# Performance work log

Hardware: AMD Instinct MI355X
Metric: run time of the kernel (lower is better)

Reference implementation:

```python
import jax, jax.numpy as jnp
import numpy as np

DIM = 512
DIM_INNER = 512
NUM_HEADS = 16
HEAD_DIM = DIM_INNER // NUM_HEADS  # 32


def setup_inputs() -> dict:
    key = jax.random.key(0)
    k1, k2, k3, k4 = jax.random.split(key, 4)
    b, n = 1, 4096
    x = jax.random.normal(k1, (b, n, DIM), dtype=jnp.float32)
    # torch nn.Linear weights, stored as (in, out) so y = x @ W (+ b)
    s_qkv = 1.0 / np.sqrt(DIM)
    W_qkv = jax.random.uniform(k2, (DIM, DIM_INNER * 3), jnp.float32, -s_qkv, s_qkv)
    W_a = jax.random.uniform(k3, (DIM, NUM_HEADS * 2), jnp.float32, -s_qkv, s_qkv)
    b_a = jax.random.uniform(k4, (NUM_HEADS * 2,), jnp.float32, -s_qkv, s_qkv)
    return {"x": x, "W_qkv": W_qkv, "W_a": W_a, "b_a": b_a}


def _gate_loop(q, k, v, a):
    # q,k,v: (bh, n, d) float32; a: (bh, n, 1, 1) complex64
    kv = jnp.einsum('bnd,bne->bnde', k, v).astype(jnp.complex64)  # (bh, n, d, d)

    def binop(ei, ej):
        a_i, kv_i = ei
        a_j, kv_j = ej
        return a_j * a_i, a_j * kv_i + kv_j

    _, kv = jax.lax.associative_scan(binop, (a, kv), axis=1)
    return jnp.einsum('bnd,bnde->bne', q, kv.real)


def reference(x, W_qkv, W_a, b_a):
    b, n, _ = x.shape
    h, d = NUM_HEADS, HEAD_DIM

    qkv = x @ W_qkv                                   # (b, n, 3*dim_inner)
    q, k, v = jnp.split(qkv, 3, axis=-1)

    def to_heads(t):  # 'b n (h d) -> (b h) n d'
        return t.reshape(b, n, h, d).transpose(0, 2, 1, 3).reshape(b * h, n, d)

    q, k, v = map(to_heads, (q, k, v))

    a_lin = x @ W_a + b_a                             # (b, n, 2h)
    a_ri = a_lin.reshape(b, n, h, 2)
    a_c = jax.lax.complex(a_ri[..., 0], a_ri[..., 1])  # (b, n, h)
    mag = jnp.abs(a_c)
    ph = jnp.angle(a_c)
    gate = jax.lax.complex(jnp.cos(ph), jnp.sin(ph)) * jax.nn.sigmoid(mag).astype(jnp.complex64)
    gate = gate.transpose(0, 2, 1).reshape(b * h, n, 1, 1)  # '(b h) n 1 1'

    out = _gate_loop(q, k, v, gate)                   # (bh, n, d)
    out = out.reshape(b, h, n, d).transpose(0, 2, 1, 3).reshape(b, n, h * d)
    # out_proj is Identity since dim_inner == dim
    return out
```

## Files before the change

kernel.cpp:

```cpp
#include <hip/hip_runtime.h>
#include <hip/hip_bf16.h>

#define SEQ    4096
#define DIM    512
#define DIM3   1536
#define NH     16
#define HD     32
#define CHUNK  64
#define NCHUNK (SEQ / CHUNK)

typedef __attribute__((ext_vector_type(8))) short short8;
typedef __attribute__((ext_vector_type(4))) float f32x4;
typedef __attribute__((ext_vector_type(4))) unsigned short u16x4;
typedef __attribute__((ext_vector_type(4))) unsigned int u32x4;

__device__ inline unsigned short f2bf(float f) {
  unsigned u = __builtin_bit_cast(unsigned, f);
  unsigned r = (u + 0x7fff + ((u >> 16) & 1)) >> 16;
  return (unsigned short)r;
}
__device__ inline float bf2f(unsigned short b) {
  unsigned u = ((unsigned)b) << 16;
  return __builtin_bit_cast(float, u);
}

__global__ __launch_bounds__(256) void gl_cvt_gate(
    const float* __restrict__ x, const float* __restrict__ W,
    const float* __restrict__ Wa, const float* __restrict__ ba,
    unsigned short* __restrict__ xb, unsigned short* __restrict__ Wt,
    float2* __restrict__ graw) {
  __shared__ union {
    float wtile[32][33];
    struct { float xs[4][DIM]; float red[4][8][32]; } g;
  } sm;
  int b = blockIdx.x;
  if (b < 2048) {
    int i = b * 256 + threadIdx.x;
    float4 v = ((const float4*)x)[i];
    u16x4 o = {f2bf(v.x), f2bf(v.y), f2bf(v.z), f2bf(v.w)};
    ((u16x4*)xb)[i] = o;
  } else if (b < 2816) {
    b -= 2048;
    int bx = b % 48, by = b / 48;
    int tx = threadIdx.x & 31, ty = threadIdx.x >> 5;
    for (int i = ty; i < 32; i += 8)
      sm.wtile[i][tx] = W[(size_t)(by * 32 + i) * DIM3 + bx * 32 + tx];
    __syncthreads();
    for (int i = ty; i < 32; i += 8)
      Wt[(size_t)(bx * 32 + i) * DIM + by * 32 + tx] = f2bf(sm.wtile[tx][i]);
  } else {
    const int n0 = (b - 2816) * 4;
    const int tid = threadIdx.x;
    const float4* xv = (const float4*)(x + (size_t)n0 * DIM);
    float4* xsv = (float4*)&sm.g.xs[0][0];
    for (int i = tid; i < 512; i += 256) xsv[i] = xv[i];
    __syncthreads();
    const int o = tid & 31, s = tid >> 5;
    float pr[4] = {0, 0, 0, 0};
    for (int k = s * 64; k < s * 64 + 64; ++k) {
      float w = Wa[k * 32 + o];
      #pragma unroll
      for (int r = 0; r < 4; ++r) pr[r] += sm.g.xs[r][k] * w;
    }
    #pragma unroll
    for (int r = 0; r < 4; ++r) sm.g.red[r][s][o] = pr[r];
    __syncthreads();
    if (tid < 128) {
      int r = tid >> 5, oo = tid & 31;
      float acc = ba[oo];
      #pragma unroll
      for (int ss = 0; ss < 8; ++ss) acc += sm.g.red[r][ss][oo];
      sm.g.red[r][0][oo] = acc;
    }
    __syncthreads();
    if (tid < 64) {
      int r = tid >> 4, hh = tid & 15;
      float re = sm.g.red[r][0][2 * hh], im = sm.g.red[r][0][2 * hh + 1];
      float mag = sqrtf(re * re + im * im);
      float lml = -log1pf(expf(-mag));
      float ph = atan2f(im, re);
      graw[(size_t)hh * SEQ + n0 + r] = make_float2(lml, ph);
    }
  }
}

#define GBM 128
#define GBN 128
#define GBK 64
__global__ __launch_bounds__(256) void gl_gemm_mfma(
    const unsigned short* __restrict__ A, const unsigned short* __restrict__ Bt,
    unsigned short* __restrict__ C) {
  __shared__ unsigned short As[2][GBM * GBK];
  __shared__ unsigned short Bs[2][GBM * GBK];
  const int tid = threadIdx.x;
  const int id = blockIdx.x;
  const int tile = (id & 7) * 48 + (id >> 3);
  const int by = tile / 12, bx = tile % 12;
  const int row0 = by * GBM, col0 = bx * GBN;
  const int wid = tid >> 6, lane = tid & 63;
  const int wr = wid >> 1, wc = wid & 1;
  const int lr = lane & 15, lg = lane >> 4;

  auto stage = [&](int buf, int t) {
    const int k0 = t * GBK;
    #pragma unroll
    for (int i = 0; i < 4; ++i) {
      int byteoff = i * 4096 + tid * 16;
      int row = byteoff >> 7;
      int logslot = ((byteoff >> 4) & 7) ^ (row & 7);
      const unsigned short* gp = A + (size_t)(row0 + row) * DIM + k0 + logslot * 8;
      __builtin_amdgcn_global_load_lds(
          (const __attribute__((address_space(1))) void*)gp,
          (__attribute__((address_space(3))) void*)((char*)As[buf] + byteoff),
          16, 0, 0);
    }
    #pragma unroll
    for (int i = 0; i < 4; ++i) {
      int byteoff = i * 4096 + tid * 16;
      int row = byteoff >> 7;
      int logslot = ((byteoff >> 4) & 7) ^ (row & 7);
      const unsigned short* gp = Bt + (size_t)(col0 + row) * DIM + k0 + logslot * 8;
      __builtin_amdgcn_global_load_lds(
          (const __attribute__((address_space(1))) void*)gp,
          (__attribute__((address_space(3))) void*)((char*)Bs[buf] + byteoff),
          16, 0, 0);
    }
  };

  f32x4 acc[4][4] = {};
  stage(0, 0);

  #pragma unroll
  for (int t = 0; t < 8; ++t) {
    const int p = t & 1;
    if (t < 7) {
      stage(p ^ 1, t + 1);
      asm volatile("s_waitcnt vmcnt(8)" ::: "memory");
    } else {
      asm volatile("s_waitcnt vmcnt(0)" ::: "memory");
    }
    __syncthreads();
    const char* AsB = (const char*)As[p];
    const char* BsB = (const char*)Bs[p];
    #pragma unroll
    for (int ks = 0; ks < 2; ++ks) {
      short8 af[4], bfr[4];
      #pragma unroll
      for (int m = 0; m < 4; ++m) {
        int row = wr * 64 + m * 16 + lr;
        int ps = (ks * 4 + lg) ^ (row & 7);
        af[m] = *(const short8*)(AsB + row * 128 + ps * 16);
      }
      #pragma unroll
      for (int n = 0; n < 4; ++n) {
        int col = wc * 64 + n * 16 + lr;
        int ps = (ks * 4 + lg) ^ (col & 7);
        bfr[n] = *(const short8*)(BsB + col * 128 + ps * 16);
      }
      #pragma unroll
      for (int m = 0; m < 4; ++m)
        #pragma unroll
        for (int n = 0; n < 4; ++n)
          acc[m][n] = __builtin_amdgcn_mfma_f32_16x16x32_bf16(
              af[m], bfr[n], acc[m][n], 0, 0, 0);
    }
    __syncthreads();
  }

  #pragma unroll
  for (int m = 0; m < 4; ++m)
    #pragma unroll
    for (int n = 0; n < 4; ++n) {
      int grow0 = row0 + wr * 64 + m * 16 + lg * 4;
      int gcol = col0 + wc * 64 + n * 16 + lr;
      #pragma unroll
      for (int j = 0; j < 4; ++j)
        C[(size_t)(grow0 + j) * DIM3 + gcol] = f2bf(acc[m][n][j]);
    }
}

__global__ __launch_bounds__(128) void gl_pass1(
    const unsigned short* __restrict__ qkv, const float2* __restrict__ graw,
    float2* __restrict__ LmPh, float* __restrict__ SLre,
    float* __restrict__ SLim, float2* __restrict__ Aprod) {
  const int b = blockIdx.x;
  const int c = b & (NCHUNK - 1), h = b >> 6;
  const int tid = threadIdx.x, w = tid >> 6, lane = tid & 63;
  const int lr = lane & 15, lg = lane >> 4;
  const int n0 = c * CHUNK;
  __shared__ float2 lmph[CHUNK];

  float2 g = graw[(size_t)h * SEQ + n0 + lane];
  float lm = g.x, ph = g.y;
  #pragma unroll
  for (int off = 1; off < 64; off <<= 1) {
    float a = __shfl_up(lm, off), p = __shfl_up(ph, off);
    if (lane >= off) { lm += a; ph += p; }
  }
  if (w == 0) {
    LmPh[(size_t)h * SEQ + n0 + lane] = make_float2(lm, ph);
    lmph[lane] = make_float2(lm, ph);
    if (lane == 63) {
      float e = __expf(lm);
      Aprod[h * NCHUNK + c] = make_float2(e * __cosf(ph), e * __sinf(ph));
    }
  }
  __syncthreads();
  const float2 end = lmph[63];

  const size_t rowb = (size_t)n0 * DIM3 + h * HD;
  f32x4 acc[2][2] = {};
  #pragma unroll
  for (int ks = 0; ks < 2; ++ks) {
    const int jb = ks * 32 + lg * 8;
    float wv[8];
    #pragma unroll
    for (int jj = 0; jj < 8; ++jj) {
      float2 lp = lmph[jb + jj];
      float e = __expf(end.x - lp.x);
      float an = end.y - lp.y;
      wv[jj] = e * (w == 0 ? __cosf(an) : __sinf(an));
    }
    short8 afr[2], bfr[2];
    #pragma unroll
    for (int mt = 0; mt < 2; ++mt) {
      int d = mt * 16 + lr;
      unsigned u0, u1, u2, u3;
      #define LD_KW(q) ((unsigned)f2bf(bf2f(qkv[rowb + (size_t)(jb + 2*(q)) * DIM3 + DIM + d]) * wv[2*(q)]) | \
                        ((unsigned)f2bf(bf2f(qkv[rowb + (size_t)(jb + 2*(q)+1) * DIM3 + DIM + d]) * wv[2*(q)+1]) << 16))
      u0 = LD_KW(0); u1 = LD_KW(1); u2 = LD_KW(2); u3 = LD_KW(3);
      #undef LD_KW
      u32x4 t = {u0, u1, u2, u3};
      afr[mt] = __builtin_bit_cast(short8, t);
    }
    #pragma unroll
    for (int nt = 0; nt < 2; ++nt) {
      int e_ = nt * 16 + lr;
      unsigned u0, u1, u2, u3;
      #define LD_V(q) ((unsigned)qkv[rowb + (size_t)(jb + 2*(q)) * DIM3 + 2*DIM + e_] | \
                       ((unsigned)qkv[rowb + (size_t)(jb + 2*(q)+1) * DIM3 + 2*DIM + e_] << 16))
      u0 = LD_V(0); u1 = LD_V(1); u2 = LD_V(2); u3 = LD_V(3);
      #undef LD_V
      u32x4 t = {u0, u1, u2, u3};
      bfr[nt] = __builtin_bit_cast(short8, t);
    }
    #pragma unroll
    for (int mt = 0; mt < 2; ++mt)
      #pragma unroll
      for (int nt = 0; nt < 2; ++nt)
        acc[mt][nt] = __builtin_amdgcn_mfma_f32_16x16x32_bf16(
            afr[mt], bfr[nt], acc[mt][nt], 0, 0, 0);
  }
  float* dst = (w == 0) ? SLre : SLim;
  const size_t base = (size_t)(h * NCHUNK + c) * (HD * HD);
  #pragma unroll
  for (int mt = 0; mt < 2; ++mt)
    #pragma unroll
    for (int nt = 0; nt < 2; ++nt)
      #pragma unroll
      for (int r = 0; r < 4; ++r) {
        int d = mt * 16 + lg * 4 + r, e_ = nt * 16 + lr;
        dst[base + d * HD + e_] = acc[mt][nt][r];
      }
}

__global__ __launch_bounds__(128) void gl_scan_chunks(
    const float* __restrict__ SLre, const float* __restrict__ SLim,
    const float2* __restrict__ Aprod, float2* __restrict__ Sin) {
  const int h = blockIdx.x >> 3;
  const int oct = blockIdx.x & 7;
  const size_t hb = (size_t)h * NCHUNK * (HD * HD) + oct * 128 + threadIdx.x;
  const float2* AP = Aprod + h * NCHUNK;
  float2 s = make_float2(0.f, 0.f);
  for (int cg = 0; cg < NCHUNK; cg += 8) {
    float lre[8], lim[8];
    float2 a[8];
    #pragma unroll
    for (int j = 0; j < 8; ++j) {
      size_t off = hb + (size_t)(cg + j) * (HD * HD);
      lre[j] = SLre[off];
      lim[j] = SLim[off];
      a[j] = AP[cg + j];
    }
    #pragma unroll
    for (int j = 0; j < 8; ++j) {
      Sin[hb + (size_t)(cg + j) * (HD * HD)] = s;
      float re = s.x, im = s.y;
      s.x = a[j].x * re - a[j].y * im + lre[j];
      s.y = a[j].x * im + a[j].y * re + lim[j];
    }
  }
}

__global__ __launch_bounds__(128) void gl_pass2(
    const unsigned short* __restrict__ qkv, const float2* __restrict__ LmPh,
    const float2* __restrict__ Sin, float* __restrict__ out) {
  const int b = blockIdx.x;
  const int c = b & (NCHUNK - 1), h = b >> 6;
  const int tid = threadIdx.x, w = tid >> 6, lane = tid & 63;
  const int lr = lane & 15, lg = lane >> 4;
  const int n0 = c * CHUNK;
  __shared__ float2 lmph[CHUNK];
  __shared__ unsigned Pp[32][68];
  if (tid < 64) lmph[tid] = LmPh[(size_t)h * SEQ + n0 + tid];
  __syncthreads();

  const size_t rowb = (size_t)n0 * DIM3 + h * HD;
  short8 kf[2], qf[4];
  #pragma unroll
  for (int mt = 0; mt < 2; ++mt) {
    int j = (2 * w + mt) * 16 + lr;
    kf[mt] = *(const short8*)(qkv + rowb + (size_t)j * DIM3 + DIM + lg * 8);
  }
  #pragma unroll
  for (int nt = 0; nt < 4; ++nt) {
    int n = nt * 16 + lr;
    qf[nt] = *(const short8*)(qkv + rowb + (size_t)n * DIM3 + lg * 8);
  }
  f32x4 pacc[2][4] = {};
  #pragma unroll
  for (int mt = 0; mt < 2; ++mt)
    #pragma unroll
    for (int nt = 0; nt < 4; ++nt)
      pacc[mt][nt] = __builtin_amdgcn_mfma_f32_16x16x32_bf16(
          kf[mt], qf[nt], pacc[mt][nt], 0, 0, 0);

  #pragma unroll
  for (int mt = 0; mt < 2; ++mt) {
    int jt = 2 * w + mt;
    #pragma unroll
    for (int r2 = 0; r2 < 2; ++r2) {
      int j0 = jt * 16 + lg * 4 + 2 * r2;
      float2 lj0 = lmph[j0], lj1 = lmph[j0 + 1];
      #pragma unroll
      for (int nt = 0; nt < 4; ++nt) {
        int n = nt * 16 + lr;
        float2 ln = lmph[n];
        float w0 = (j0 <= n) ? __expf(ln.x - lj0.x) * __cosf(ln.y - lj0.y) : 0.f;
        float w1 = (j0 + 1 <= n) ? __expf(ln.x - lj1.x) * __cosf(ln.y - lj1.y) : 0.f;
        Pp[jt * 8 + lg * 2 + r2][n] =
            (unsigned)f2bf(pacc[mt][nt][2 * r2] * w0) |
            ((unsigned)f2bf(pacc[mt][nt][2 * r2 + 1] * w1) << 16);
      }
    }
  }
  __syncthreads();

  const size_t soff = (size_t)(h * NCHUNK + c) * (HD * HD);
  short8 sre[2], sim[2];
  #pragma unroll
  for (int nt = 0; nt < 2; ++nt) {
    int e_ = nt * 16 + lr;
    unsigned ur[4], ui[4];
    #pragma unroll
    for (int q = 0; q < 4; ++q) {
      float2 s0 = Sin[soff + (size_t)(lg * 8 + 2 * q) * HD + e_];
      float2 s1 = Sin[soff + (size_t)(lg * 8 + 2 * q + 1) * HD + e_];
      ur[q] = (unsigned)f2bf(s0.x) | ((unsigned)f2bf(s1.x) << 16);
      ui[q] = (unsigned)f2bf(s0.y) | ((unsigned)f2bf(s1.y) << 16);
    }
    u32x4 tr = {ur[0], ur[1], ur[2], ur[3]};
    u32x4 ti = {ui[0], ui[1], ui[2], ui[3]};
    sre[nt] = __builtin_bit_cast(short8, tr);
    sim[nt] = __builtin_bit_cast(short8, ti);
  }
  f32x4 ore[2][2] = {}, oim[2][2] = {};
  #pragma unroll
  for (int mt = 0; mt < 2; ++mt)
    #pragma unroll
    for (int nt = 0; nt < 2; ++nt) {
      ore[mt][nt] = __builtin_amdgcn_mfma_f32_16x16x32_bf16(
          qf[2 * w + mt], sre[nt], ore[mt][nt], 0, 0, 0);
      oim[mt][nt] = __builtin_amdgcn_mfma_f32_16x16x32_bf16(
          qf[2 * w + mt], sim[nt], oim[mt][nt], 0, 0, 0);
    }
  f32x4 oacc[2][2];
  #pragma unroll
  for (int mt = 0; mt < 2; ++mt)
    #pragma unroll
    for (int r = 0; r < 4; ++r) {
      int n = (2 * w + mt) * 16 + lg * 4 + r;
      float2 ln = lmph[n];
      float eg = __expf(ln.x);
      float gr = eg * __cosf(ln.y), gi = eg * __sinf(ln.y);
      oacc[mt][0][r] = gr * ore[mt][0][r] - gi * oim[mt][0][r];
      oacc[mt][1][r] = gr * ore[mt][1][r] - gi * oim[mt][1][r];
    }
  #pragma unroll
  for (int ks = 0; ks < 2; ++ks) {
    short8 pa[2];
    #pragma unroll
    for (int mt = 0; mt < 2; ++mt) {
      int n_ = (2 * w + mt) * 16 + lr;
      unsigned u0 = Pp[ks * 16 + lg * 4 + 0][n_];
      unsigned u1 = Pp[ks * 16 + lg * 4 + 1][n_];
      unsigned u2 = Pp[ks * 16 + lg * 4 + 2][n_];
      unsigned u3 = Pp[ks * 16 + lg * 4 + 3][n_];
      u32x4 t = {u0, u1, u2, u3};
      pa[mt] = __builtin_bit_cast(short8, t);
    }
    const int jb = ks * 32 + lg * 8;
    short8 vf[2];
    #pragma unroll
    for (int nt = 0; nt < 2; ++nt) {
      int e_ = nt * 16 + lr;
      unsigned u0, u1, u2, u3;
      #define LD_V(q) ((unsigned)qkv[rowb + (size_t)(jb + 2*(q)) * DIM3 + 2*DIM + e_] | \
                       ((unsigned)qkv[rowb + (size_t)(jb + 2*(q)+1) * DIM3 + 2*DIM + e_] << 16))
      u0 = LD_V(0); u1 = LD_V(1); u2 = LD_V(2); u3 = LD_V(3);
      #undef LD_V
      u32x4 t = {u0, u1, u2, u3};
      vf[nt] = __builtin_bit_cast(short8, t);
    }
    #pragma unroll
    for (int mt = 0; mt < 2; ++mt)
      #pragma unroll
      for (int nt = 0; nt < 2; ++nt)
        oacc[mt][nt] = __builtin_amdgcn_mfma_f32_16x16x32_bf16(
            pa[mt], vf[nt], oacc[mt][nt], 0, 0, 0);
  }
  #pragma unroll
  for (int mt = 0; mt < 2; ++mt)
    #pragma unroll
    for (int nt = 0; nt < 2; ++nt)
      #pragma unroll
      for (int r = 0; r < 4; ++r) {
        int n = (2 * w + mt) * 16 + lg * 4 + r;
        int e_ = nt * 16 + lr;
        out[(size_t)(n0 + n) * DIM + h * HD + e_] = oacc[mt][nt][r];
      }
}

extern "C" void kernel_launch(void* const* d_in, const int* in_sizes, int n_in,
                              void* d_out, int out_size, void* d_ws,
                              size_t ws_size, hipStream_t stream) {
  const float* x     = (const float*)d_in[0];
  const float* W_qkv = (const float*)d_in[1];
  const float* W_a   = (const float*)d_in[2];
  const float* b_a   = (const float*)d_in[3];
  float* out = (float*)d_out;

  char* ws = (char*)d_ws;
  unsigned short* qkv  = (unsigned short*)ws;
  float2* graw  = (float2*)(ws + 12582912);
  float2* LmPh  = (float2*)(ws + 13107200);
  float*  SLre  = (float*)(ws + 13631488);
  float*  SLim  = (float*)(ws + 17825792);
  float2* Aprod = (float2*)(ws + 22020096);
  float2* Sin   = (float2*)(ws + 22028288);
  unsigned short* xb = (unsigned short*)(ws + 30416896);
  unsigned short* Wt = (unsigned short*)(ws + 34611200);

  gl_cvt_gate<<<3840, 256, 0, stream>>>(x, W_qkv, W_a, b_a, xb, Wt, graw);
  gl_gemm_mfma<<<384, 256, 0, stream>>>(xb, Wt, qkv);
  gl_pass1<<<NCHUNK * NH, 128, 0, stream>>>(qkv, graw, LmPh, SLre, SLim, Aprod);
  gl_scan_chunks<<<128, 128, 0, stream>>>(SLre, SLim, Aprod, Sin);
  gl_pass2<<<NCHUNK * NH, 128, 0, stream>>>(qkv, LmPh, Sin, out);
}
```

Baseline: 51.76 us.

## Fuse x conversion into gate blocks, halve GEMM M-tile, store chunk states as packed bf16

Three changes. First, the x→bf16 conversion moves into the gate-projection blocks, which already load x, so x is read once instead of twice. Second, the QKV GEMM M-tile drops from 128 to 64, doubling the block count to 768 so more CUs stay busy, at the cost of less reuse per block. Third, the chunk-scan kernel writes inter-chunk states as bf16 pairs packed into separate real and imaginary arrays, using a cross-lane shuffle. This halves the state traffic and removes the per-load conversion in pass2, at the cost of rounding the stored states to bf16 earlier.

```diff
diff --git a/kernel.cpp b/kernel.cpp
--- a/kernel.cpp
+++ b/kernel.cpp
@@ -34,26 +34,18 @@
     struct { float xs[4][DIM]; float red[4][8][32]; } g;
   } sm;
   int b = blockIdx.x;
-  if (b < 2048) {
-    int i = b * 256 + threadIdx.x;
-    float4 v = ((const float4*)x)[i];
-    u16x4 o = {f2bf(v.x), f2bf(v.y), f2bf(v.z), f2bf(v.w)};
-    ((u16x4*)xb)[i] = o;
-  } else if (b < 2816) {
-    b -= 2048;
-    int bx = b % 48, by = b / 48;
-    int tx = threadIdx.x & 31, ty = threadIdx.x >> 5;
-    for (int i = ty; i < 32; i += 8)
-      sm.wtile[i][tx] = W[(size_t)(by * 32 + i) * DIM3 + bx * 32 + tx];
-    __syncthreads();
-    for (int i = ty; i < 32; i += 8)
-      Wt[(size_t)(bx * 32 + i) * DIM + by * 32 + tx] = f2bf(sm.wtile[tx][i]);
-  } else {
-    const int n0 = (b - 2816) * 4;
+  if (b < 1024) {
+    const int n0 = b * 4;
     const int tid = threadIdx.x;
     const float4* xv = (const float4*)(x + (size_t)n0 * DIM);
+    u16x4* xbo = (u16x4*)(xb + (size_t)n0 * DIM);
     float4* xsv = (float4*)&sm.g.xs[0][0];
-    for (int i = tid; i < 512; i += 256) xsv[i] = xv[i];
+    for (int i = tid; i < 512; i += 256) {
+      float4 v = xv[i];
+      xsv[i] = v;
+      u16x4 o = {f2bf(v.x), f2bf(v.y), f2bf(v.z), f2bf(v.w)};
+      xbo[i] = o;
+    }
     __syncthreads();
     const int o = tid & 31, s = tid >> 5;
     float pr[4] = {0, 0, 0, 0};
@@ -81,20 +73,29 @@
       float ph = atan2f(im, re);
       graw[(size_t)hh * SEQ + n0 + r] = make_float2(lml, ph);
     }
-  }
-}
-
-#define GBM 128
+  } else {
+    b -= 1024;
+    int bx = b % 48, by = b / 48;
+    int tx = threadIdx.x & 31, ty = threadIdx.x >> 5;
+    for (int i = ty; i < 32; i += 8)
+      sm.wtile[i][tx] = W[(size_t)(by * 32 + i) * DIM3 + bx * 32 + tx];
+    __syncthreads();
+    for (int i = ty; i < 32; i += 8)
+      Wt[(size_t)(bx * 32 + i) * DIM + by * 32 + tx] = f2bf(sm.wtile[tx][i]);
+  }
+}
+
+#define GBM 64
 #define GBN 128
 #define GBK 64
 __global__ __launch_bounds__(256) void gl_gemm_mfma(
     const unsigned short* __restrict__ A, const unsigned short* __restrict__ Bt,
     unsigned short* __restrict__ C) {
   __shared__ unsigned short As[2][GBM * GBK];
-  __shared__ unsigned short Bs[2][GBM * GBK];
+  __shared__ unsigned short Bs[2][GBN * GBK];
   const int tid = threadIdx.x;
   const int id = blockIdx.x;
-  const int tile = (id & 7) * 48 + (id >> 3);
+  const int tile = (id & 7) * 96 + (id >> 3);
   const int by = tile / 12, bx = tile % 12;
   const int row0 = by * GBM, col0 = bx * GBN;
   const int wid = tid >> 6, lane = tid & 63;
@@ -104,7 +105,7 @@
   auto stage = [&](int buf, int t) {
     const int k0 = t * GBK;
     #pragma unroll
-    for (int i = 0; i < 4; ++i) {
+    for (int i = 0; i < 2; ++i) {
       int byteoff = i * 4096 + tid * 16;
       int row = byteoff >> 7;
       int logslot = ((byteoff >> 4) & 7) ^ (row & 7);
@@ -127,7 +128,7 @@
     }
   };
 
-  f32x4 acc[4][4] = {};
+  f32x4 acc[2][4] = {};
   stage(0, 0);
 
   #pragma unroll
@@ -135,7 +136,7 @@
     const int p = t & 1;
     if (t < 7) {
       stage(p ^ 1, t + 1);
-      asm volatile("s_waitcnt vmcnt(8)" ::: "memory");
+      asm volatile("s_waitcnt vmcnt(6)" ::: "memory");
     } else {
       asm volatile("s_waitcnt vmcnt(0)" ::: "memory");
     }
@@ -144,10 +145,10 @@
     const char* BsB = (const char*)Bs[p];
     #pragma unroll
     for (int ks = 0; ks < 2; ++ks) {
-      short8 af[4], bfr[4];
-      #pragma unroll
-      for (int m = 0; m < 4; ++m) {
-        int row = wr * 64 + m * 16 + lr;
+      short8 af[2], bfr[4];
+      #pragma unroll
+      for (int m = 0; m < 2; ++m) {
+        int row = wr * 32 + m * 16 + lr;
         int ps = (ks * 4 + lg) ^ (row & 7);
         af[m] = *(const short8*)(AsB + row * 128 + ps * 16);
       }
@@ -158,7 +159,7 @@
         bfr[n] = *(const short8*)(BsB + col * 128 + ps * 16);
       }
       #pragma unroll
-      for (int m = 0; m < 4; ++m)
+      for (int m = 0; m < 2; ++m)
         #pragma unroll
         for (int n = 0; n < 4; ++n)
           acc[m][n] = __builtin_amdgcn_mfma_f32_16x16x32_bf16(
@@ -168,10 +169,10 @@
   }
 
   #pragma unroll
-  for (int m = 0; m < 4; ++m)
+  for (int m = 0; m < 2; ++m)
     #pragma unroll
     for (int n = 0; n < 4; ++n) {
-      int grow0 = row0 + wr * 64 + m * 16 + lg * 4;
+      int grow0 = row0 + wr * 32 + m * 16 + lg * 4;
       int gcol = col0 + wc * 64 + n * 16 + lr;
       #pragma unroll
       for (int j = 0; j < 4; ++j)
@@ -266,10 +267,16 @@
 
 __global__ __launch_bounds__(128) void gl_scan_chunks(
     const float* __restrict__ SLre, const float* __restrict__ SLim,
-    const float2* __restrict__ Aprod, float2* __restrict__ Sin) {
+    const float2* __restrict__ Aprod, unsigned* __restrict__ SinPre,
+    unsigned* __restrict__ SinPim) {
   const int h = blockIdx.x >> 3;
   const int oct = blockIdx.x & 7;
-  const size_t hb = (size_t)h * NCHUNK * (HD * HD) + oct * 128 + threadIdx.x;
+  const int tid = threadIdx.x;
+  const int elem = oct * 128 + tid;
+  const int e = elem & 31;
+  const int qp = elem >> 6;
+  const bool lo = !(tid & 32);
+  const size_t hb = (size_t)h * NCHUNK * (HD * HD) + elem;
   const float2* AP = Aprod + h * NCHUNK;
   float2 s = make_float2(0.f, 0.f);
   for (int cg = 0; cg < NCHUNK; cg += 8) {
@@ -284,7 +291,13 @@
     }
     #pragma unroll
     for (int j = 0; j < 8; ++j) {
-      Sin[hb + (size_t)(cg + j) * (HD * HD)] = s;
+      float px = __shfl_xor(s.x, 32);
+      float py = __shfl_xor(s.y, 32);
+      if (lo) {
+        size_t wo = (size_t)(h * NCHUNK + cg + j) * 512 + qp * 32 + e;
+        SinPre[wo] = (unsigned)f2bf(s.x) | ((unsigned)f2bf(px) << 16);
+        SinPim[wo] = (unsigned)f2bf(s.y) | ((unsigned)f2bf(py) << 16);
+      }
       float re = s.x, im = s.y;
       s.x = a[j].x * re - a[j].y * im + lre[j];
       s.y = a[j].x * im + a[j].y * re + lim[j];
@@ -294,7 +307,8 @@
 
 __global__ __launch_bounds__(128) void gl_pass2(
     const unsigned short* __restrict__ qkv, const float2* __restrict__ LmPh,
-    const float2* __restrict__ Sin, float* __restrict__ out) {
+    const unsigned* __restrict__ SinPre, const unsigned* __restrict__ SinPim,
+    float* __restrict__ out) {
   const int b = blockIdx.x;
   const int c = b & (NCHUNK - 1), h = b >> 6;
   const int tid = threadIdx.x, w = tid >> 6, lane = tid & 63;
@@ -346,7 +360,7 @@
   }
   __syncthreads();
 
-  const size_t soff = (size_t)(h * NCHUNK + c) * (HD * HD);
+  const size_t s512 = (size_t)(h * NCHUNK + c) * 512;
   short8 sre[2], sim[2];
   #pragma unroll
   for (int nt = 0; nt < 2; ++nt) {
@@ -354,10 +368,8 @@
     unsigned ur[4], ui[4];
     #pragma unroll
     for (int q = 0; q < 4; ++q) {
-      float2 s0 = Sin[soff + (size_t)(lg * 8 + 2 * q) * HD + e_];
-      float2 s1 = Sin[soff + (size_t)(lg * 8 + 2 * q + 1) * HD + e_];
-      ur[q] = (unsigned)f2bf(s0.x) | ((unsigned)f2bf(s1.x) << 16);
-      ui[q] = (unsigned)f2bf(s0.y) | ((unsigned)f2bf(s1.y) << 16);
+      ur[q] = SinPre[s512 + (size_t)(lg * 4 + q) * 32 + e_];
+      ui[q] = SinPim[s512 + (size_t)(lg * 4 + q) * 32 + e_];
     }
     u32x4 tr = {ur[0], ur[1], ur[2], ur[3]};
     u32x4 ti = {ui[0], ui[1], ui[2], ui[3]};
@@ -447,13 +459,14 @@
   float*  SLre  = (float*)(ws + 13631488);
   float*  SLim  = (float*)(ws + 17825792);
   float2* Aprod = (float2*)(ws + 22020096);
-  float2* Sin   = (float2*)(ws + 22028288);
-  unsigned short* xb = (unsigned short*)(ws + 30416896);
-  unsigned short* Wt = (unsigned short*)(ws + 34611200);
-
-  gl_cvt_gate<<<3840, 256, 0, stream>>>(x, W_qkv, W_a, b_a, xb, Wt, graw);
-  gl_gemm_mfma<<<384, 256, 0, stream>>>(xb, Wt, qkv);
+  unsigned* SinPre = (unsigned*)(ws + 22028288);
+  unsigned* SinPim = (unsigned*)(ws + 24125440);
+  unsigned short* xb = (unsigned short*)(ws + 26222592);
+  unsigned short* Wt = (unsigned short*)(ws + 30416896);
+
+  gl_cvt_gate<<<1792, 256, 0, stream>>>(x, W_qkv, W_a, b_a, xb, Wt, graw);
+  gl_gemm_mfma<<<768, 256, 0, stream>>>(xb, Wt, qkv);
   gl_pass1<<<NCHUNK * NH, 128, 0, stream>>>(qkv, graw, LmPh, SLre, SLim, Aprod);
-  gl_scan_chunks<<<128, 128, 0, stream>>>(SLre, SLim, Aprod, Sin);
-  gl_pass2<<<NCHUNK * NH, 128, 0, stream>>>(qkv, LmPh, Sin, out);
-}
+  gl_scan_chunks<<<128, 128, 0, stream>>>(SLre, SLim, Aprod, SinPre, SinPim);
+  gl_pass2<<<NCHUNK * NH, 128, 0, stream>>>(qkv, LmPh, SinPre, SinPim, out);
+}
```

Measured after the change: 52.84 us. +2.1%, slower.
